# Optimization experiments

Hardware: AMD Instinct MI355X
Metric: run time of the kernel (lower is better)

## Reference

```python
import jax, jax.numpy as jnp
import numpy as np

D = 256       # input_dim == output_dim (required by residual + attn Linears)
HN = 4        # num_node_heads
HT = 4        # num_type_heads
N = 50000     # nodes per node type (A and B)
E = 300000    # edges per relation (both relations are B -> A)
R = 2         # num relations incident on dst type A
ALPHA = 0.5
SLOPE = 0.01  # torch F.leaky_relu default
EPS = 1e-9


def _normalize(x):
    # torch: x / max(norm(x, dim=1, keepdim=True), 1e-9); for 2D/last-dim feature
    n = jnp.linalg.norm(x, axis=-1, keepdims=True)
    return x / jnp.maximum(n, EPS)


def setup_inputs() -> dict:
    key = jax.random.key(0)
    ks = jax.random.split(key, 16)
    s = jnp.float32(0.05)
    return {
        "h_A": jax.random.normal(ks[0], (N, D), jnp.float32),
        "h_B": jax.random.normal(ks[1], (N, D), jnp.float32),
        "src0": jax.random.randint(ks[2], (E,), 0, N),
        "dst0": jax.random.randint(ks[3], (E,), 0, N),
        "src1": jax.random.randint(ks[4], (E,), 0, N),
        "dst1": jax.random.randint(ks[5], (E,), 0, N),
        "node_W": jax.random.normal(ks[6], (2, D, D), jnp.float32) * s,
        "node_b": jnp.zeros((2, D), jnp.float32),
        "edge_W": jax.random.normal(ks[7], (R, D, D), jnp.float32) * s,
        "edge_b": jnp.zeros((R, D), jnp.float32),
        "srcA_W": jax.random.normal(ks[8], (R, D, HN), jnp.float32) * s,
        "srcA_b": jnp.zeros((R, HN), jnp.float32),
        "dstA_W": jax.random.normal(ks[9], (R, D, HN), jnp.float32) * s,
        "dstA_b": jnp.zeros((R, HN), jnp.float32),
        "semS_W": jax.random.normal(ks[10], (R, D, HT), jnp.float32) * s,
        "semS_b": jnp.zeros((R, HT), jnp.float32),
        "semD_W": jax.random.normal(ks[11], (R, D, HT), jnp.float32) * s,
        "semD_b": jnp.zeros((R, HT), jnp.float32),
        "relA_W": jax.random.normal(ks[12], (R, D, HT), jnp.float32) * s,
        "relA_b": jnp.zeros((R, HT), jnp.float32),
        "rel_emb": jax.random.normal(ks[13], (R, D), jnp.float32) * jnp.float32(1.414),
    }


def _relation_z(h_src, h_dst, We, be, Wn, bn, Ws, bs, Wd, bd, src, dst):
    """Per-relation GAT-style message passing with DGL edge_softmax semantics."""
    hs = h_src @ We + be                    # edge_linear[e_id](h_src)  [N,D]
    hd = h_dst @ Wn + bn                    # node_linear[dst_id](h_dst) [N,D]
    a_src = hs @ Ws + bs                    # src_attn  [N,HN]
    a_dst = hd @ Wd + bd                    # dst_attn  [N,HN]
    a = jax.nn.leaky_relu(a_src[src] + a_dst[dst], SLOPE)   # u_add_v  [E,HN]
    # edge_softmax: segmented softmax over in-edges of each dst node
    m = jax.ops.segment_max(a, dst, num_segments=N)
    ex = jnp.exp(a - m[dst])
    denom = jax.ops.segment_sum(ex, dst, num_segments=N)
    w = ex / denom[dst]                     # [E,HN]
    v = hs.reshape(N, HN, D // HN)
    msg = v[src] * w[:, :, None]            # u_mul_e   [E,HN,D/HN]
    z = jax.ops.segment_sum(msg, dst, num_segments=N)       # fn.sum
    return z.reshape(N, D)


def reference(h_A, h_B, src0, dst0, src1, dst1, node_W, node_b, edge_W, edge_b,
              srcA_W, srcA_b, dstA_W, dstA_b, semS_W, semS_b, semD_W, semD_b,
              relA_W, relA_b, rel_emb):
    # Graph: relations (B -r0-> A) and (B -r1-> A); node ids: A=0, B=1.
    z0 = _relation_z(h_B, h_A, edge_W[0], edge_b[0], node_W[0], node_b[0],
                     srcA_W[0], srcA_b[0], dstA_W[0], dstA_b[0], src0, dst0)
    z1 = _relation_z(h_B, h_A, edge_W[1], edge_b[1], node_W[0], node_b[0],
                     srcA_W[1], srcA_b[1], dstA_W[1], dstA_b[1], src1, dst1)
    z_src = jnp.stack([z0, z1], axis=1)     # cross_reducer='stack' [N,R,D]

    # --- dst type A: semantic + relation attention fusion ---
    z_dst = h_A @ node_W[0] + node_b[0]
    sem = (jnp.einsum('nrd,rdh->nrh', _normalize(z_src), semS_W) + semS_b
           + jnp.einsum('nd,rdh->nrh', _normalize(z_dst), semD_W) + semD_b)  # [N,R,HT]
    sem = jax.nn.softmax(jax.nn.leaky_relu(sem, SLOPE), axis=1)
    rel = jnp.einsum('rd,rdh->rh', rel_emb, relA_W) + relA_b   # [R,HT], node-invariant
    rel = jax.nn.softmax(jax.nn.leaky_relu(rel, SLOPE), axis=0)
    attn = ALPHA * sem + (1.0 - ALPHA) * rel[None]             # [N,R,HT]

    zc = (z_src.reshape(N, R, HT, D // HT) * attn[..., None]).reshape(N, R, D).sum(axis=1)
    out_A = _normalize(jax.nn.gelu(zc + h_A, approximate=False))

    # --- node type B: no incoming edges -> fallback branch ---
    out_B = _normalize(jax.nn.gelu(h_B @ node_W[1] + node_b[1] + h_B, approximate=False))
    return jnp.stack([out_A, out_B])        # [2,N,D]
```

## Files before the change

### kernel.cpp

```cpp
#include <hip/hip_runtime.h>
#include <math.h>

#define D 256
#define HN 4
#define HT 4

typedef __bf16 bf16x8 __attribute__((ext_vector_type(8)));
typedef float  f32x16 __attribute__((ext_vector_type(16)));

__device__ __forceinline__ float lrelu(float x){ return x > 0.f ? x : 0.01f*x; }
__device__ __forceinline__ float gelu_exact(float x){ return 0.5f*x*(1.f+erff(x*0.70710678118654752f)); }

__device__ __forceinline__ float wred_sum(float v){
#pragma unroll
  for (int o = 32; o > 0; o >>= 1) v += __shfl_xor(v, o);
  return v;
}
__device__ __forceinline__ float4 wred_sum4(float4 v){
  v.x = wred_sum(v.x); v.y = wred_sum(v.y); v.z = wred_sum(v.z); v.w = wred_sum(v.w);
  return v;
}

#define ACC4(p, s, w) do { (p).x = fmaf((s),(w).x,(p).x); (p).y = fmaf((s),(w).y,(p).y); \
                           (p).z = fmaf((s),(w).z,(p).z); (p).w = fmaf((s),(w).w,(p).w); } while(0)

__global__ void wt_setup(const float* __restrict__ nodeW, const float* __restrict__ edgeW,
                         __bf16* __restrict__ WtHi, __bf16* __restrict__ WtLo)
{
  int idx = blockIdx.x*256 + threadIdx.x;
  int mat = idx >> 16;
  int e   = idx & 65535;
  int n   = e & 255;
  int k   = e >> 8;
  const float* src = (mat==0)? nodeW : (mat==1)? nodeW+65536 : (mat==2)? edgeW : edgeW+65536;
  float x = src[k*256 + n];
  __bf16 hi = (__bf16)x;
  __bf16 lo = (__bf16)(x - (float)hi);
  size_t o = (size_t)mat*65536 + (size_t)n*256 + k;
  WtHi[o] = hi;
  WtLo[o] = lo;
}

__device__ __forceinline__ void cvt8(const float4 a, const float4 b, bf16x8& h, bf16x8& l){
  float v0=a.x,v1=a.y,v2=a.z,v3=a.w,v4=b.x,v5=b.y,v6=b.z,v7=b.w;
  __bf16 t;
  t=(__bf16)v0; h[0]=t; l[0]=(__bf16)(v0-(float)t);
  t=(__bf16)v1; h[1]=t; l[1]=(__bf16)(v1-(float)t);
  t=(__bf16)v2; h[2]=t; l[2]=(__bf16)(v2-(float)t);
  t=(__bf16)v3; h[3]=t; l[3]=(__bf16)(v3-(float)t);
  t=(__bf16)v4; h[4]=t; l[4]=(__bf16)(v4-(float)t);
  t=(__bf16)v5; h[5]=t; l[5]=(__bf16)(v5-(float)t);
  t=(__bf16)v6; h[6]=t; l[6]=(__bf16)(v6-(float)t);
  t=(__bf16)v7; h[7]=t; l[7]=(__bf16)(v7-(float)t);
}

__global__ __launch_bounds__(256) void gemm_mfma(
    const float* __restrict__ A, const __bf16* __restrict__ WtHi, const __bf16* __restrict__ WtLo,
    const float* __restrict__ bias, float* __restrict__ C, int M)
{
  __shared__ __align__(16) char smem[33024];
  const int tid  = threadIdx.x;
  const int bm   = blockIdx.x * 128;
  const int bn   = blockIdx.y * 128;
  const int lane = tid & 63;
  const int wid  = tid >> 6;
  const int wm   = wid >> 1, wn = wid & 1;

  f32x16 acc[2][2] = {};

  const int sm_row = tid >> 1;
  const int sk     = (tid & 1) * 16;
  int arow = bm + sm_row; if (arow >= M) arow = M - 1;
  const float*  gA  = A    + (size_t)arow*256 + sk;
  const __bf16* gWh = WtHi + (size_t)(bn + sm_row)*256 + sk;
  const __bf16* gWl = WtLo + (size_t)(bn + sm_row)*256 + sk;
  const int s0  = (tid & 1) * 2;
  const int wrO = sm_row * 16;

  float4 f0,f1,f2,f3; uint4 u0,u1,u2,u3;
  f0 = *(const float4*)(gA + 0);  f1 = *(const float4*)(gA + 4);
  f2 = *(const float4*)(gA + 8);  f3 = *(const float4*)(gA + 12);
  u0 = *(const uint4*)(gWh + 0);  u1 = *(const uint4*)(gWh + 8);
  u2 = *(const uint4*)(gWl + 0);  u3 = *(const uint4*)(gWl + 8);

  for (int it = 0; it < 8; ++it) {
    bf16x8 h0,h1,l0,l1;
    cvt8(f0, f1, h0, l0);
    cvt8(f2, f3, h1, l1);
    __syncthreads();
    *(bf16x8*)(smem +         s0   *2064 + wrO) = h0;
    *(bf16x8*)(smem +        (s0+1)*2064 + wrO) = h1;
    *(bf16x8*)(smem +  8256 + s0   *2064 + wrO) = l0;
    *(bf16x8*)(smem +  8256 +(s0+1)*2064 + wrO) = l1;
    *(uint4*)(smem + 16512 + s0   *2064 + wrO) = u0;
    *(uint4*)(smem + 16512 +(s0+1)*2064 + wrO) = u1;
    *(uint4*)(smem + 24768 + s0   *2064 + wrO) = u2;
    *(uint4*)(smem + 24768 +(s0+1)*2064 + wrO) = u3;
    if (it < 7) {
      int k0 = (it+1)*32;
      f0 = *(const float4*)(gA + k0 + 0);  f1 = *(const float4*)(gA + k0 + 4);
      f2 = *(const float4*)(gA + k0 + 8);  f3 = *(const float4*)(gA + k0 + 12);
      u0 = *(const uint4*)(gWh + k0);      u1 = *(const uint4*)(gWh + k0 + 8);
      u2 = *(const uint4*)(gWl + k0);      u3 = *(const uint4*)(gWl + k0 + 8);
    }
    __syncthreads();
#pragma unroll
    for (int ks = 0; ks < 2; ++ks) {
      const int fo = (ks*2 + (lane>>5))*2064 + (lane&31)*16;
      bf16x8 aH0 = *(const bf16x8*)(smem +         fo + (wm*64    )*16);
      bf16x8 aH1 = *(const bf16x8*)(smem +         fo + (wm*64+32 )*16);
      bf16x8 aL0 = *(const bf16x8*)(smem +  8256 + fo + (wm*64    )*16);
      bf16x8 aL1 = *(const bf16x8*)(smem +  8256 + fo + (wm*64+32 )*16);
      bf16x8 bH0 = *(const bf16x8*)(smem + 16512 + fo + (wn*64    )*16);
      bf16x8 bH1 = *(const bf16x8*)(smem + 16512 + fo + (wn*64+32 )*16);
      bf16x8 bL0 = *(const bf16x8*)(smem + 24768 + fo + (wn*64    )*16);
      bf16x8 bL1 = *(const bf16x8*)(smem + 24768 + fo + (wn*64+32 )*16);
      acc[0][0] = __builtin_amdgcn_mfma_f32_32x32x16_bf16(aH0,bH0,acc[0][0],0,0,0);
      acc[0][0] = __builtin_amdgcn_mfma_f32_32x32x16_bf16(aH0,bL0,acc[0][0],0,0,0);
      acc[0][0] = __builtin_amdgcn_mfma_f32_32x32x16_bf16(aL0,bH0,acc[0][0],0,0,0);
      acc[0][1] = __builtin_amdgcn_mfma_f32_32x32x16_bf16(aH0,bH1,acc[0][1],0,0,0);
      acc[0][1] = __builtin_amdgcn_mfma_f32_32x32x16_bf16(aH0,bL1,acc[0][1],0,0,0);
      acc[0][1] = __builtin_amdgcn_mfma_f32_32x32x16_bf16(aL0,bH1,acc[0][1],0,0,0);
      acc[1][0] = __builtin_amdgcn_mfma_f32_32x32x16_bf16(aH1,bH0,acc[1][0],0,0,0);
      acc[1][0] = __builtin_amdgcn_mfma_f32_32x32x16_bf16(aH1,bL0,acc[1][0],0,0,0);
      acc[1][0] = __builtin_amdgcn_mfma_f32_32x32x16_bf16(aL1,bH0,acc[1][0],0,0,0);
      acc[1][1] = __builtin_amdgcn_mfma_f32_32x32x16_bf16(aH1,bH1,acc[1][1],0,0,0);
      acc[1][1] = __builtin_amdgcn_mfma_f32_32x32x16_bf16(aH1,bL1,acc[1][1],0,0,0);
      acc[1][1] = __builtin_amdgcn_mfma_f32_32x32x16_bf16(aL1,bH1,acc[1][1],0,0,0);
    }
  }

  const int col = bn + wn*64 + (lane&31);
#pragma unroll
  for (int fn = 0; fn < 2; ++fn) {
    float bval = bias[col + fn*32];
#pragma unroll
    for (int fm = 0; fm < 2; ++fm) {
      int rbase = bm + wm*64 + fm*32 + 4*(lane>>5);
#pragma unroll
      for (int r = 0; r < 16; ++r) {
        int row = rbase + (r&3) + 8*(r>>2);
        if (row < M) C[(size_t)row*256 + col + fn*32] = acc[fm][fn][r] + bval;
      }
    }
  }
}

__global__ __launch_bounds__(256) void attn_vec_kernel(
    const float* __restrict__ hs0, const float* __restrict__ hs1,
    const float* __restrict__ hd,
    const float* __restrict__ srcA_W, const float* __restrict__ srcA_b,
    const float* __restrict__ dstA_W, const float* __restrict__ dstA_b,
    float* __restrict__ as0, float* __restrict__ as1,
    float* __restrict__ ad0, float* __restrict__ ad1, int N)
{
  int n = blockIdx.x*4 + (threadIdx.x >> 6);
  if (n >= N) return;
  int lane = threadIdx.x & 63;
  int d0 = lane << 2;
  const float4* Ws = (const float4*)srcA_W;
  const float4* Wd = (const float4*)dstA_W;
  float4 r0 = ((const float4*)hs0)[(size_t)n*64 + lane];
  float4 r1 = ((const float4*)hs1)[(size_t)n*64 + lane];
  float4 rd = ((const float4*)hd )[(size_t)n*64 + lane];
  float4 p0 = make_float4(0,0,0,0), p1 = make_float4(0,0,0,0);
  float4 q0 = make_float4(0,0,0,0), q1 = make_float4(0,0,0,0);
  float4 w;
  w = Ws[d0+0]; ACC4(p0, r0.x, w);
  w = Ws[d0+1]; ACC4(p0, r0.y, w);
  w = Ws[d0+2]; ACC4(p0, r0.z, w);
  w = Ws[d0+3]; ACC4(p0, r0.w, w);
  w = Ws[256+d0+0]; ACC4(p1, r1.x, w);
  w = Ws[256+d0+1]; ACC4(p1, r1.y, w);
  w = Ws[256+d0+2]; ACC4(p1, r1.z, w);
  w = Ws[256+d0+3]; ACC4(p1, r1.w, w);
  w = Wd[d0+0]; ACC4(q0, rd.x, w);
  w = Wd[d0+1]; ACC4(q0, rd.y, w);
  w = Wd[d0+2]; ACC4(q0, rd.z, w);
  w = Wd[d0+3]; ACC4(q0, rd.w, w);
  w = Wd[256+d0+0]; ACC4(q1, rd.x, w);
  w = Wd[256+d0+1]; ACC4(q1, rd.y, w);
  w = Wd[256+d0+2]; ACC4(q1, rd.z, w);
  w = Wd[256+d0+3]; ACC4(q1, rd.w, w);
  p0 = wred_sum4(p0); p1 = wred_sum4(p1); q0 = wred_sum4(q0); q1 = wred_sum4(q1);
  if (lane == 0) {
    float4 b;
    b = *(const float4*)(srcA_b + 0);
    ((float4*)as0)[n] = make_float4(p0.x+b.x, p0.y+b.y, p0.z+b.z, p0.w+b.w);
    b = *(const float4*)(srcA_b + 4);
    ((float4*)as1)[n] = make_float4(p1.x+b.x, p1.y+b.y, p1.z+b.z, p1.w+b.w);
    b = *(const float4*)(dstA_b + 0);
    ((float4*)ad0)[n] = make_float4(q0.x+b.x, q0.y+b.y, q0.z+b.z, q0.w+b.w);
    b = *(const float4*)(dstA_b + 4);
    ((float4*)ad1)[n] = make_float4(q1.x+b.x, q1.y+b.y, q1.z+b.z, q1.w+b.w);
  }
}

__global__ void rel_kernel(const float* __restrict__ rel_emb, const float* __restrict__ relA_W,
                           const float* __restrict__ relA_b, float* __restrict__ rel_out)
{
  int t = threadIdx.x;
  if (t < 8) {
    int r = t >> 2, h = t & 3;
    float s = relA_b[r*4+h];
    for (int d = 0; d < 256; ++d)
      s = fmaf(rel_emb[r*256+d], relA_W[(size_t)(r*256+d)*4+h], s);
    s = lrelu(s);
    float other = __shfl_xor(s, 4);
    float mm = fmaxf(s, other);
    float e  = expf(s - mm), eo = expf(other - mm);
    rel_out[r*4+h] = 0.5f * e / (e + eo);
  }
}

__global__ void zero_int(int* p, int n){
  int i = blockIdx.x*blockDim.x + threadIdx.x;
  if (i < n) p[i] = 0;
}

__global__ void hist_kernel(const int* __restrict__ dst0, const int* __restrict__ dst1,
                            int* c0, int* c1, int E){
  int e = blockIdx.x*256 + threadIdx.x;
  if (e < E) { atomicAdd(&c0[dst0[e]], 1); atomicAdd(&c1[dst1[e]], 1); }
}

__global__ __launch_bounds__(1024) void scan1(const int* __restrict__ cnt0, const int* __restrict__ cnt1,
                                              int* __restrict__ rp0, int* __restrict__ rp1,
                                              int* __restrict__ part0, int* __restrict__ part1, int n){
  const int* cnt = blockIdx.y ? cnt1 : cnt0;
  int* excl = blockIdx.y ? rp1 : rp0;
  int* part = blockIdx.y ? part1 : part0;
  __shared__ int sm[1024];
  int tid = threadIdx.x;
  int gid = blockIdx.x*1024 + tid;
  int v = (gid < n) ? cnt[gid] : 0;
  sm[tid] = v; __syncthreads();
  for (int off = 1; off < 1024; off <<= 1){
    int t = sm[tid];
    if (tid >= off) t += sm[tid-off];
    __syncthreads();
    sm[tid] = t; __syncthreads();
  }
  if (gid < n) excl[gid] = sm[tid] - v;
  if (tid == 1023) part[blockIdx.x] = sm[1023];
}

__global__ void scan2(int* part0, int* part1, int nchunk, int* tot0, int* tot1){
  if (threadIdx.x == 0 && blockIdx.x == 0){
    int run = 0;
    for (int i = 0; i < nchunk; ++i){ int t = part0[i]; part0[i] = run; run += t; }
    *tot0 = run;
    run = 0;
    for (int i = 0; i < nchunk; ++i){ int t = part1[i]; part1[i] = run; run += t; }
    *tot1 = run;
  }
}

__global__ __launch_bounds__(1024) void scan3(int* __restrict__ rp0, int* __restrict__ rp1,
                                              int* __restrict__ cur0, int* __restrict__ cur1,
                                              const int* __restrict__ part0, const int* __restrict__ part1, int n){
  int* rp  = blockIdx.y ? rp1 : rp0;
  int* cur = blockIdx.y ? cur1 : cur0;
  const int* part = blockIdx.y ? part1 : part0;
  int gid = blockIdx.x*1024 + threadIdx.x;
  if (gid < n){ int v = rp[gid] + part[blockIdx.x]; rp[gid] = v; cur[gid] = v; }
}

__global__ void scatter_kernel(const int* __restrict__ src0, const int* __restrict__ dst0,
                               int* cur0, int* __restrict__ csr0,
                               const int* __restrict__ src1, const int* __restrict__ dst1,
                               int* cur1, int* __restrict__ csr1, int E){
  int e = blockIdx.x*256 + threadIdx.x;
  if (e < E){
    int p = atomicAdd(&cur0[dst0[e]], 1); csr0[p] = src0[e];
    p = atomicAdd(&cur1[dst1[e]], 1); csr1[p] = src1[e];
  }
}

__device__ __forceinline__ float4 agg_one(
    const int* __restrict__ rp, const int* __restrict__ csr,
    const float* __restrict__ as, const float* __restrict__ ad,
    const float* __restrict__ hs, float* __restrict__ exb,
    int n, int lane, int h)
{
  int start = rp[n];
  int cnt   = rp[n+1] - start;
  float4 acc = make_float4(0,0,0,0);
  if (cnt == 0) return acc;
  float4 adv = *(const float4*)(ad + (size_t)n*4);
  float4 ssum = make_float4(0,0,0,0);
  for (int i = lane; i < cnt; i += 64) {
    int s = csr[start+i];
    float4 a = *(const float4*)(as + (size_t)s*4);
    float4 e;
    e.x = __expf(lrelu(a.x+adv.x));
    e.y = __expf(lrelu(a.y+adv.y));
    e.z = __expf(lrelu(a.z+adv.z));
    e.w = __expf(lrelu(a.w+adv.w));
    *(float4*)(exb + (size_t)(start+i)*4) = e;
    ssum.x += e.x; ssum.y += e.y; ssum.z += e.z; ssum.w += e.w;
  }
  ssum = wred_sum4(ssum);
  asm volatile("s_waitcnt vmcnt(0)" ::: "memory");
  float sh  = h==0?ssum.x : h==1?ssum.y : h==2?ssum.z : ssum.w;
  float invh = 1.f / sh;
  const volatile float* exv = exb;
  const float4* hsv = (const float4*)hs;
  int i = 0;
  for (; i+2 <= cnt; i += 2) {
    int sa = csr[start+i], sb = csr[start+i+1];
    float wa = exv[(size_t)(start+i)*4 + h];
    float wb = exv[(size_t)(start+i+1)*4 + h];
    float4 va = hsv[(size_t)sa*64 + lane];
    float4 vb = hsv[(size_t)sb*64 + lane];
    acc.x = fmaf(va.x,wa,acc.x); acc.y = fmaf(va.y,wa,acc.y);
    acc.z = fmaf(va.z,wa,acc.z); acc.w = fmaf(va.w,wa,acc.w);
    acc.x = fmaf(vb.x,wb,acc.x); acc.y = fmaf(vb.y,wb,acc.y);
    acc.z = fmaf(vb.z,wb,acc.z); acc.w = fmaf(vb.w,wb,acc.w);
  }
  if (i < cnt) {
    int sa = csr[start+i];
    float wa = exv[(size_t)(start+i)*4 + h];
    float4 va = hsv[(size_t)sa*64 + lane];
    acc.x = fmaf(va.x,wa,acc.x); acc.y = fmaf(va.y,wa,acc.y);
    acc.z = fmaf(va.z,wa,acc.z); acc.w = fmaf(va.w,wa,acc.w);
  }
  acc.x *= invh; acc.y *= invh; acc.z *= invh; acc.w *= invh;
  return acc;
}

__device__ __forceinline__ void sm2(float s0, float s1, float r0, float r1, float& o0, float& o1){
  float mm = fmaxf(s0, s1);
  float e0 = expf(s0-mm), e1 = expf(s1-mm);
  float inv = 1.f/(e0+e1);
  o0 = fmaf(0.5f*e0, inv, r0);
  o1 = fmaf(0.5f*e1, inv, r1);
}

__global__ __launch_bounds__(256) void aggregate_fused(
    const int* __restrict__ rp0, const int* __restrict__ csr0,
    const float* __restrict__ as0, const float* __restrict__ ad0,
    const float* __restrict__ hs0, float* __restrict__ exb0,
    const int* __restrict__ rp1, const int* __restrict__ csr1,
    const float* __restrict__ as1, const float* __restrict__ ad1,
    const float* __restrict__ hs1, float* __restrict__ exb1,
    float* __restrict__ hd_io, const float* __restrict__ hA,
    const float* __restrict__ semS_W, const float* __restrict__ semS_b,
    const float* __restrict__ semD_W, const float* __restrict__ semD_b,
    const float* __restrict__ relw, int N)
{
  int n = blockIdx.x*4 + (threadIdx.x >> 6);
  if (n >= N) return;
  int lane = threadIdx.x & 63;
  int h = lane >> 4;

  float4 a0 = agg_one(rp0, csr0, as0, ad0, hs0, exb0, n, lane, h);
  float4 a1 = agg_one(rp1, csr1, as1, ad1, hs1, exb1, n, lane, h);

  int d0 = lane << 2;
  float4 ad = ((float4*)hd_io)[(size_t)n*64 + lane];
  float4 ha = ((const float4*)hA)[(size_t)n*64 + lane];
  float nz0 = wred_sum(a0.x*a0.x + a0.y*a0.y + a0.z*a0.z + a0.w*a0.w);
  float nz1 = wred_sum(a1.x*a1.x + a1.y*a1.y + a1.z*a1.z + a1.w*a1.w);
  float nzd = wred_sum(ad.x*ad.x + ad.y*ad.y + ad.z*ad.z + ad.w*ad.w);
  float i0  = 1.f / fmaxf(sqrtf(nz0), 1e-9f);
  float i1  = 1.f / fmaxf(sqrtf(nz1), 1e-9f);
  float idn = 1.f / fmaxf(sqrtf(nzd), 1e-9f);
  const float4* WS = (const float4*)semS_W;
  const float4* WD = (const float4*)semD_W;
  float4 p0 = make_float4(0,0,0,0), p1 = make_float4(0,0,0,0);
  float4 q0 = make_float4(0,0,0,0), q1 = make_float4(0,0,0,0);
  float4 w;
  w = WS[d0+0]; ACC4(p0, a0.x, w);
  w = WS[d0+1]; ACC4(p0, a0.y, w);
  w = WS[d0+2]; ACC4(p0, a0.z, w);
  w = WS[d0+3]; ACC4(p0, a0.w, w);
  w = WS[256+d0+0]; ACC4(p1, a1.x, w);
  w = WS[256+d0+1]; ACC4(p1, a1.y, w);
  w = WS[256+d0+2]; ACC4(p1, a1.z, w);
  w = WS[256+d0+3]; ACC4(p1, a1.w, w);
  w = WD[d0+0]; ACC4(q0, ad.x, w);
  w = WD[d0+1]; ACC4(q0, ad.y, w);
  w = WD[d0+2]; ACC4(q0, ad.z, w);
  w = WD[d0+3]; ACC4(q0, ad.w, w);
  w = WD[256+d0+0]; ACC4(q1, ad.x, w);
  w = WD[256+d0+1]; ACC4(q1, ad.y, w);
  w = WD[256+d0+2]; ACC4(q1, ad.z, w);
  w = WD[256+d0+3]; ACC4(q1, ad.w, w);
  p0 = wred_sum4(p0); p1 = wred_sum4(p1); q0 = wred_sum4(q0); q1 = wred_sum4(q1);
  float4 sb0 = *(const float4*)(semS_b + 0);
  float4 sb1 = *(const float4*)(semS_b + 4);
  float4 db0 = *(const float4*)(semD_b + 0);
  float4 db1 = *(const float4*)(semD_b + 4);
  float4 s0, s1;
  s0.x = lrelu(p0.x*i0 + sb0.x + q0.x*idn + db0.x);
  s0.y = lrelu(p0.y*i0 + sb0.y + q0.y*idn + db0.y);
  s0.z = lrelu(p0.z*i0 + sb0.z + q0.z*idn + db0.z);
  s0.w = lrelu(p0.w*i0 + sb0.w + q0.w*idn + db0.w);
  s1.x = lrelu(p1.x*i1 + sb1.x + q1.x*idn + db1.x);
  s1.y = lrelu(p1.y*i1 + sb1.y + q1.y*idn + db1.y);
  s1.z = lrelu(p1.z*i1 + sb1.z + q1.z*idn + db1.z);
  s1.w = lrelu(p1.w*i1 + sb1.w + q1.w*idn + db1.w);
  float4 at0, at1;
  sm2(s0.x, s1.x, relw[0], relw[4], at0.x, at1.x);
  sm2(s0.y, s1.y, relw[1], relw[5], at0.y, at1.y);
  sm2(s0.z, s1.z, relw[2], relw[6], at0.z, at1.z);
  sm2(s0.w, s1.w, relw[3], relw[7], at0.w, at1.w);
  float w0 = h==0 ? at0.x : h==1 ? at0.y : h==2 ? at0.z : at0.w;
  float w1 = h==0 ? at1.x : h==1 ? at1.y : h==2 ? at1.z : at1.w;
  float4 x;
  x.x = fmaf(a0.x, w0, fmaf(a1.x, w1, ha.x));
  x.y = fmaf(a0.y, w0, fmaf(a1.y, w1, ha.y));
  x.z = fmaf(a0.z, w0, fmaf(a1.z, w1, ha.z));
  x.w = fmaf(a0.w, w0, fmaf(a1.w, w1, ha.w));
  float4 g;
  g.x = gelu_exact(x.x); g.y = gelu_exact(x.y); g.z = gelu_exact(x.z); g.w = gelu_exact(x.w);
  float ng = wred_sum(g.x*g.x + g.y*g.y + g.z*g.z + g.w*g.w);
  float inv = 1.f / fmaxf(sqrtf(ng), 1e-9f);
  g.x *= inv; g.y *= inv; g.z *= inv; g.w *= inv;
  ((float4*)hd_io)[(size_t)n*64 + lane] = g;
}

__global__ __launch_bounds__(256) void fusionB_kernel(float* __restrict__ outB,
                                                      const float* __restrict__ hB, int N)
{
  int n = blockIdx.x*4 + (threadIdx.x >> 6);
  if (n >= N) return;
  int lane = threadIdx.x & 63;
  float4 x = ((float4*)outB)[(size_t)n*64 + lane];
  float4 b = ((const float4*)hB)[(size_t)n*64 + lane];
  x.x += b.x; x.y += b.y; x.z += b.z; x.w += b.w;
  float4 g;
  g.x = gelu_exact(x.x); g.y = gelu_exact(x.y); g.z = gelu_exact(x.z); g.w = gelu_exact(x.w);
  float ng = wred_sum(g.x*g.x + g.y*g.y + g.z*g.z + g.w*g.w);
  float inv = 1.f / fmaxf(sqrtf(ng), 1e-9f);
  g.x *= inv; g.y *= inv; g.z *= inv; g.w *= inv;
  ((float4*)outB)[(size_t)n*64 + lane] = g;
}

extern "C" void kernel_launch(void* const* d_in, const int* in_sizes, int n_in,
                              void* d_out, int out_size, void* d_ws, size_t ws_size,
                              hipStream_t stream)
{
  const float* hA     = (const float*)d_in[0];
  const float* hB     = (const float*)d_in[1];
  const int*   src0   = (const int*)d_in[2];
  const int*   dst0   = (const int*)d_in[3];
  const int*   src1   = (const int*)d_in[4];
  const int*   dst1   = (const int*)d_in[5];
  const float* node_W = (const float*)d_in[6];
  const float* node_b = (const float*)d_in[7];
  const float* edge_W = (const float*)d_in[8];
  const float* edge_b = (const float*)d_in[9];
  const float* srcA_W = (const float*)d_in[10];
  const float* srcA_b = (const float*)d_in[11];
  const float* dstA_W = (const float*)d_in[12];
  const float* dstA_b = (const float*)d_in[13];
  const float* semS_W = (const float*)d_in[14];
  const float* semS_b = (const float*)d_in[15];
  const float* semD_W = (const float*)d_in[16];
  const float* semD_b = (const float*)d_in[17];
  const float* relA_W = (const float*)d_in[18];
  const float* relA_b = (const float*)d_in[19];
  const float* rel_emb= (const float*)d_in[20];

  const int N = in_sizes[0] / D;
  const int E = in_sizes[2];

  float* out  = (float*)d_out;
  float* outA = out;
  float* outB = out + (size_t)N*D;

  float* w = (float*)d_ws;
  float* hs0  = w; w += (size_t)N*D;
  float* hs1  = w; w += (size_t)N*D;
  float* exb0 = w; w += (size_t)E*HN;
  float* exb1 = w; w += (size_t)E*HN;
  float* as0  = w; w += (size_t)N*HN;
  float* as1  = w; w += (size_t)N*HN;
  float* ad0  = w; w += (size_t)N*HN;
  float* ad1  = w; w += (size_t)N*HN;
  float* relw = w; w += 16;
  __bf16* WtHi = (__bf16*)w; w += 131072;
  __bf16* WtLo = (__bf16*)w; w += 131072;
  int* ip   = (int*)w;
  int* cnt0 = ip; ip += N;
  int* cnt1 = ip; ip += N;
  int* rp0  = ip; ip += N+1;
  int* rp1  = ip; ip += N+1;
  int* cur0 = ip; ip += N;
  int* cur1 = ip; ip += N;
  int* part0= ip; ip += 256;
  int* part1= ip; ip += 256;
  int* csr0 = ip; ip += E;
  int* csr1 = ip; ip += E;

  const int nwb = (N + 3) / 4;
  dim3 ggrid((N + 127)/128, 2);

  wt_setup<<<1024, 256, 0, stream>>>(node_W, edge_W, WtHi, WtLo);

  gemm_mfma<<<ggrid, 256, 0, stream>>>(hA, WtHi + 0*65536, WtLo + 0*65536, node_b,       outA, N);
  gemm_mfma<<<ggrid, 256, 0, stream>>>(hB, WtHi + 2*65536, WtLo + 2*65536, edge_b,       hs0,  N);
  gemm_mfma<<<ggrid, 256, 0, stream>>>(hB, WtHi + 3*65536, WtLo + 3*65536, edge_b + D,   hs1,  N);
  gemm_mfma<<<ggrid, 256, 0, stream>>>(hB, WtHi + 1*65536, WtLo + 1*65536, node_b + D,   outB, N);

  attn_vec_kernel<<<nwb, 256, 0, stream>>>(hs0, hs1, outA, srcA_W, srcA_b, dstA_W, dstA_b,
                                           as0, as1, ad0, ad1, N);
  rel_kernel<<<1, 64, 0, stream>>>(rel_emb, relA_W, relA_b, relw);

  zero_int<<<(2*N + 255)/256, 256, 0, stream>>>(cnt0, 2*N);
  hist_kernel<<<(E + 255)/256, 256, 0, stream>>>(dst0, dst1, cnt0, cnt1, E);
  const int nchunk = (N + 1023)/1024;
  dim3 sgrid(nchunk, 2);
  scan1<<<sgrid, 1024, 0, stream>>>(cnt0, cnt1, rp0, rp1, part0, part1, N);
  scan2<<<1, 64, 0, stream>>>(part0, part1, nchunk, rp0 + N, rp1 + N);
  scan3<<<sgrid, 1024, 0, stream>>>(rp0, rp1, cur0, cur1, part0, part1, N);
  scatter_kernel<<<(E + 255)/256, 256, 0, stream>>>(src0, dst0, cur0, csr0,
                                                    src1, dst1, cur1, csr1, E);

  aggregate_fused<<<nwb, 256, 0, stream>>>(rp0, csr0, as0, ad0, hs0, exb0,
                                           rp1, csr1, as1, ad1, hs1, exb1,
                                           outA, hA, semS_W, semS_b, semD_W, semD_b,
                                           relw, N);

  fusionB_kernel<<<nwb, 256, 0, stream>>>(outB, hB, N);
}
```

Before: 702.2 us.

## Merge four GEMMs into one launch and split aggregation per relation across waves

The four projection GEMMs are folded into one launch, using blockIdx.z to pick input, weight, bias and output. The aggregation kernel drops the two-pass edge softmax and its exb scratch buffer. Each wave now computes the exp weight per edge inline and accumulates the weighted sum and the normalizer in a single pass. Each relation gets its own wave, two nodes per block, and results are combined through LDS. This removes the global scratch writes, halves the serial per-wave work and raises parallelism, but drops the max-subtraction safeguard (which the old code also lacked) and adds a block barrier.

After: 629.6 us. 10.3% less time.

```diff
diff --git a/kernel.cpp b/kernel.cpp
--- a/kernel.cpp
+++ b/kernel.cpp
@@ -54,10 +54,21 @@
   t=(__bf16)v7; h[7]=t; l[7]=(__bf16)(v7-(float)t);
 }
 
-__global__ __launch_bounds__(256) void gemm_mfma(
-    const float* __restrict__ A, const __bf16* __restrict__ WtHi, const __bf16* __restrict__ WtLo,
-    const float* __restrict__ bias, float* __restrict__ C, int M)
-{
+__global__ __launch_bounds__(256) void gemm_mfma4(
+    const float* __restrict__ hA, const float* __restrict__ hB,
+    const __bf16* __restrict__ WtHi, const __bf16* __restrict__ WtLo,
+    const float* __restrict__ node_b, const float* __restrict__ edge_b,
+    float* __restrict__ outA, float* __restrict__ hs0,
+    float* __restrict__ hs1, float* __restrict__ outB, int M)
+{
+  const int z = blockIdx.z;
+  const float* A    = (z==0)? hA : hB;
+  const int    mat  = (z==0)? 0 : (z==1)? 2 : (z==2)? 3 : 1;
+  const float* bias = (z==0)? node_b : (z==1)? edge_b : (z==2)? edge_b+256 : node_b+256;
+  float*       C    = (z==0)? outA : (z==1)? hs0 : (z==2)? hs1 : outB;
+  const __bf16* Wh  = WtHi + (size_t)mat*65536;
+  const __bf16* Wl  = WtLo + (size_t)mat*65536;
+
   __shared__ __align__(16) char smem[33024];
   const int tid  = threadIdx.x;
   const int bm   = blockIdx.x * 128;
@@ -71,9 +82,9 @@
   const int sm_row = tid >> 1;
   const int sk     = (tid & 1) * 16;
   int arow = bm + sm_row; if (arow >= M) arow = M - 1;
-  const float*  gA  = A    + (size_t)arow*256 + sk;
-  const __bf16* gWh = WtHi + (size_t)(bn + sm_row)*256 + sk;
-  const __bf16* gWl = WtLo + (size_t)(bn + sm_row)*256 + sk;
+  const float*  gA  = A  + (size_t)arow*256 + sk;
+  const __bf16* gWh = Wh + (size_t)(bn + sm_row)*256 + sk;
+  const __bf16* gWl = Wl + (size_t)(bn + sm_row)*256 + sk;
   const int s0  = (tid & 1) * 2;
   const int wrO = sm_row * 16;
 
@@ -277,58 +288,6 @@
   }
 }
 
-__device__ __forceinline__ float4 agg_one(
-    const int* __restrict__ rp, const int* __restrict__ csr,
-    const float* __restrict__ as, const float* __restrict__ ad,
-    const float* __restrict__ hs, float* __restrict__ exb,
-    int n, int lane, int h)
-{
-  int start = rp[n];
-  int cnt   = rp[n+1] - start;
-  float4 acc = make_float4(0,0,0,0);
-  if (cnt == 0) return acc;
-  float4 adv = *(const float4*)(ad + (size_t)n*4);
-  float4 ssum = make_float4(0,0,0,0);
-  for (int i = lane; i < cnt; i += 64) {
-    int s = csr[start+i];
-    float4 a = *(const float4*)(as + (size_t)s*4);
-    float4 e;
-    e.x = __expf(lrelu(a.x+adv.x));
-    e.y = __expf(lrelu(a.y+adv.y));
-    e.z = __expf(lrelu(a.z+adv.z));
-    e.w = __expf(lrelu(a.w+adv.w));
-    *(float4*)(exb + (size_t)(start+i)*4) = e;
-    ssum.x += e.x; ssum.y += e.y; ssum.z += e.z; ssum.w += e.w;
-  }
-  ssum = wred_sum4(ssum);
-  asm volatile("s_waitcnt vmcnt(0)" ::: "memory");
-  float sh  = h==0?ssum.x : h==1?ssum.y : h==2?ssum.z : ssum.w;
-  float invh = 1.f / sh;
-  const volatile float* exv = exb;
-  const float4* hsv = (const float4*)hs;
-  int i = 0;
-  for (; i+2 <= cnt; i += 2) {
-    int sa = csr[start+i], sb = csr[start+i+1];
-    float wa = exv[(size_t)(start+i)*4 + h];
-    float wb = exv[(size_t)(start+i+1)*4 + h];
-    float4 va = hsv[(size_t)sa*64 + lane];
-    float4 vb = hsv[(size_t)sb*64 + lane];
-    acc.x = fmaf(va.x,wa,acc.x); acc.y = fmaf(va.y,wa,acc.y);
-    acc.z = fmaf(va.z,wa,acc.z); acc.w = fmaf(va.w,wa,acc.w);
-    acc.x = fmaf(vb.x,wb,acc.x); acc.y = fmaf(vb.y,wb,acc.y);
-    acc.z = fmaf(vb.z,wb,acc.z); acc.w = fmaf(vb.w,wb,acc.w);
-  }
-  if (i < cnt) {
-    int sa = csr[start+i];
-    float wa = exv[(size_t)(start+i)*4 + h];
-    float4 va = hsv[(size_t)sa*64 + lane];
-    acc.x = fmaf(va.x,wa,acc.x); acc.y = fmaf(va.y,wa,acc.y);
-    acc.z = fmaf(va.z,wa,acc.z); acc.w = fmaf(va.w,wa,acc.w);
-  }
-  acc.x *= invh; acc.y *= invh; acc.z *= invh; acc.w *= invh;
-  return acc;
-}
-
 __device__ __forceinline__ void sm2(float s0, float s1, float r0, float r1, float& o0, float& o1){
   float mm = fmaxf(s0, s1);
   float e0 = expf(s0-mm), e1 = expf(s1-mm);
@@ -337,26 +296,80 @@
   o1 = fmaf(0.5f*e1, inv, r1);
 }
 
-__global__ __launch_bounds__(256) void aggregate_fused(
+__global__ __launch_bounds__(256) void aggregate_fused2(
     const int* __restrict__ rp0, const int* __restrict__ csr0,
     const float* __restrict__ as0, const float* __restrict__ ad0,
-    const float* __restrict__ hs0, float* __restrict__ exb0,
+    const float* __restrict__ hs0,
     const int* __restrict__ rp1, const int* __restrict__ csr1,
     const float* __restrict__ as1, const float* __restrict__ ad1,
-    const float* __restrict__ hs1, float* __restrict__ exb1,
+    const float* __restrict__ hs1,
     float* __restrict__ hd_io, const float* __restrict__ hA,
     const float* __restrict__ semS_W, const float* __restrict__ semS_b,
     const float* __restrict__ semD_W, const float* __restrict__ semD_b,
     const float* __restrict__ relw, int N)
 {
-  int n = blockIdx.x*4 + (threadIdx.x >> 6);
-  if (n >= N) return;
-  int lane = threadIdx.x & 63;
-  int h = lane >> 4;
-
-  float4 a0 = agg_one(rp0, csr0, as0, ad0, hs0, exb0, n, lane, h);
-  float4 a1 = agg_one(rp1, csr1, as1, ad1, hs1, exb1, n, lane, h);
-
+  __shared__ float4 a1_lds[2][64];
+  const int tid    = threadIdx.x;
+  const int lane   = tid & 63;
+  const int wid    = tid >> 6;
+  const int locn   = wid >> 1;
+  const int rel    = wid & 1;
+  const int n      = blockIdx.x*2 + locn;
+  const int h      = lane >> 4;
+  const bool active = (n < N);
+
+  float4 acc = make_float4(0.f,0.f,0.f,0.f);
+  if (active) {
+    const int*   rp  = rel ? rp1  : rp0;
+    const int*   csr = rel ? csr1 : csr0;
+    const float* as  = rel ? as1  : as0;
+    const float* ad  = rel ? ad1  : ad0;
+    const float* hs  = rel ? hs1  : hs0;
+    int start = rp[n];
+    int cnt   = rp[n+1] - start;
+    if (cnt > 0) {
+      float adh = ad[(size_t)n*4 + h];
+      const float4* hsv = (const float4*)hs;
+      float ssum = 0.f;
+      int i = 0;
+      for (; i+4 <= cnt; i += 4) {
+        int s0 = csr[start+i], s1 = csr[start+i+1], s2 = csr[start+i+2], s3 = csr[start+i+3];
+        float w0 = __expf(lrelu(as[(size_t)s0*4+h] + adh));
+        float w1 = __expf(lrelu(as[(size_t)s1*4+h] + adh));
+        float w2 = __expf(lrelu(as[(size_t)s2*4+h] + adh));
+        float w3 = __expf(lrelu(as[(size_t)s3*4+h] + adh));
+        float4 v0 = hsv[(size_t)s0*64 + lane];
+        float4 v1 = hsv[(size_t)s1*64 + lane];
+        float4 v2 = hsv[(size_t)s2*64 + lane];
+        float4 v3 = hsv[(size_t)s3*64 + lane];
+        acc.x = fmaf(v0.x,w0,acc.x); acc.y = fmaf(v0.y,w0,acc.y);
+        acc.z = fmaf(v0.z,w0,acc.z); acc.w = fmaf(v0.w,w0,acc.w);
+        acc.x = fmaf(v1.x,w1,acc.x); acc.y = fmaf(v1.y,w1,acc.y);
+        acc.z = fmaf(v1.z,w1,acc.z); acc.w = fmaf(v1.w,w1,acc.w);
+        acc.x = fmaf(v2.x,w2,acc.x); acc.y = fmaf(v2.y,w2,acc.y);
+        acc.z = fmaf(v2.z,w2,acc.z); acc.w = fmaf(v2.w,w2,acc.w);
+        acc.x = fmaf(v3.x,w3,acc.x); acc.y = fmaf(v3.y,w3,acc.y);
+        acc.z = fmaf(v3.z,w3,acc.z); acc.w = fmaf(v3.w,w3,acc.w);
+        ssum += w0 + w1 + w2 + w3;
+      }
+      for (; i < cnt; ++i) {
+        int s = csr[start+i];
+        float wv = __expf(lrelu(as[(size_t)s*4+h] + adh));
+        float4 v = hsv[(size_t)s*64 + lane];
+        acc.x = fmaf(v.x,wv,acc.x); acc.y = fmaf(v.y,wv,acc.y);
+        acc.z = fmaf(v.z,wv,acc.z); acc.w = fmaf(v.w,wv,acc.w);
+        ssum += wv;
+      }
+      float inv = 1.f / ssum;
+      acc.x *= inv; acc.y *= inv; acc.z *= inv; acc.w *= inv;
+    }
+  }
+  if (rel == 1) a1_lds[locn][lane] = acc;
+  __syncthreads();
+  if (rel == 1 || !active) return;
+
+  float4 a0 = acc;
+  float4 a1 = a1_lds[locn][lane];
   int d0 = lane << 2;
   float4 ad = ((float4*)hd_io)[(size_t)n*64 + lane];
   float4 ha = ((const float4*)hA)[(size_t)n*64 + lane];
@@ -474,8 +487,6 @@
   float* w = (float*)d_ws;
   float* hs0  = w; w += (size_t)N*D;
   float* hs1  = w; w += (size_t)N*D;
-  float* exb0 = w; w += (size_t)E*HN;
-  float* exb1 = w; w += (size_t)E*HN;
   float* as0  = w; w += (size_t)N*HN;
   float* as1  = w; w += (size_t)N*HN;
   float* ad0  = w; w += (size_t)N*HN;
@@ -496,14 +507,12 @@
   int* csr1 = ip; ip += E;
 
   const int nwb = (N + 3) / 4;
-  dim3 ggrid((N + 127)/128, 2);
 
   wt_setup<<<1024, 256, 0, stream>>>(node_W, edge_W, WtHi, WtLo);
 
-  gemm_mfma<<<ggrid, 256, 0, stream>>>(hA, WtHi + 0*65536, WtLo + 0*65536, node_b,       outA, N);
-  gemm_mfma<<<ggrid, 256, 0, stream>>>(hB, WtHi + 2*65536, WtLo + 2*65536, edge_b,       hs0,  N);
-  gemm_mfma<<<ggrid, 256, 0, stream>>>(hB, WtHi + 3*65536, WtLo + 3*65536, edge_b + D,   hs1,  N);
-  gemm_mfma<<<ggrid, 256, 0, stream>>>(hB, WtHi + 1*65536, WtLo + 1*65536, node_b + D,   outB, N);
+  dim3 ggrid((N + 127)/128, 2, 4);
+  gemm_mfma4<<<ggrid, 256, 0, stream>>>(hA, hB, WtHi, WtLo, node_b, edge_b,
+                                        outA, hs0, hs1, outB, N);
 
   attn_vec_kernel<<<nwb, 256, 0, stream>>>(hs0, hs1, outA, srcA_W, srcA_b, dstA_W, dstA_b,
                                            as0, as1, ad0, ad1, N);
@@ -519,10 +528,10 @@
   scatter_kernel<<<(E + 255)/256, 256, 0, stream>>>(src0, dst0, cur0, csr0,
                                                     src1, dst1, cur1, csr1, E);
 
-  aggregate_fused<<<nwb, 256, 0, stream>>>(rp0, csr0, as0, ad0, hs0, exb0,
-                                           rp1, csr1, as1, ad1, hs1, exb1,
-                                           outA, hA, semS_W, semS_b, semD_W, semD_b,
-                                           relw, N);
+  aggregate_fused2<<<(N + 1)/2, 256, 0, stream>>>(rp0, csr0, as0, ad0, hs0,
+                                                  rp1, csr1, as1, ad1, hs1,
+                                                  outA, hA, semS_W, semS_b, semD_W, semD_b,
+                                                  relw, N);
 
   fusionB_kernel<<<nwb, 256, 0, stream>>>(outB, hB, N);
 }
```
